# Performance work log

Measured on AMD Instinct MI355X. Metric: run time of the kernel, lower is better.

## Reference

```python
import jax, jax.numpy as jnp
import numpy as np

LMBDA = 1000.0
GAMMA = 1.0  # resolvent_gamma


def setup_inputs() -> dict:
    key = jax.random.key(0)
    k = jax.random.split(key, 6)
    B, K, N, D = 16, 128, 8000, 256
    return {
        "evals_a": jax.random.uniform(k[0], (B, K), dtype=jnp.float32) + 1e-3,
        "pinv_a": jax.random.normal(k[1], (B, K, N), dtype=jnp.float32),
        "descr_a": jax.random.normal(k[2], (B, D, N), dtype=jnp.float32),
        "evals_b": jax.random.uniform(k[3], (B, K), dtype=jnp.float32) + 1e-3,
        "pinv_b": jax.random.normal(k[4], (B, K, N), dtype=jnp.float32),
        "descr_b": jax.random.normal(k[5], (B, D, N), dtype=jnp.float32),
    }


def _compute_mask(evals_a, evals_b, gamma):
    # evals_*: [B, K]. Per-batch normalization by joint max, then resolvent mask.
    scale = jnp.maximum(evals_a.max(axis=-1), evals_b.max(axis=-1))[:, None]
    ga = jnp.power(evals_a / scale, gamma)[:, None, :]  # [B, 1, K]
    gb = jnp.power(evals_b / scale, gamma)[:, :, None]  # [B, K, 1]
    M_re = gb / (gb * gb + 1.0) - ga / (ga * ga + 1.0)
    M_im = 1.0 / (gb * gb + 1.0) - 1.0 / (ga * ga + 1.0)
    return M_re * M_re + M_im * M_im  # [B, K, K]


def _compute_fmap(sdescr_a, sdescr_b, mask, lmbda):
    # sdescr_*: [B, D, K]; mask: [B, K, K]
    AA_aa = jnp.einsum("bdk,bdl->bkl", sdescr_a, sdescr_a)  # [B, K, K]
    AA_ba = jnp.einsum("bdk,bdl->bkl", sdescr_b, sdescr_a)  # [B, K, K]
    K = mask.shape[-1]
    eye = jnp.eye(K, dtype=mask.dtype)
    # Per row i: (AA_aa + lmbda * diag(mask[b, i, :]))^{-1} AA_ba[b, i, :]^T
    A = AA_aa[:, None, :, :] + lmbda * mask[..., None] * eye  # [B, K, K, K]
    Cab = jnp.linalg.solve(A, AA_ba[..., None])[..., 0]  # [B, K, K], row i = solution
    return Cab


def reference(evals_a, pinv_a, descr_a, evals_b, pinv_b, descr_b):
    # spectral descriptor projection: (pinv @ descr^T)^T -> [B, D, K]
    sdescr_a = jnp.einsum("bkn,bdn->bdk", pinv_a, descr_a)
    sdescr_b = jnp.einsum("bkn,bdn->bdk", pinv_b, descr_b)
    mask_ab = _compute_mask(evals_a, evals_b, GAMMA)
    fmap_12 = _compute_fmap(sdescr_a, sdescr_b, mask_ab, LMBDA)
    mask_ba = _compute_mask(evals_b, evals_a, GAMMA)
    fmap_21 = _compute_fmap(sdescr_b, sdescr_a, mask_ba, LMBDA)
    return (fmap_12, fmap_21)
```

## Files before the change

### kernel.cpp

```cpp
#include <hip/hip_runtime.h>

#define BB 16
#define KD 128
#define ND 8000
#define DD 256
#define LMB 1000.0f

typedef __attribute__((ext_vector_type(8))) short bf16x8;
typedef __attribute__((ext_vector_type(4))) short bf16x4;
typedef __attribute__((ext_vector_type(4))) float f32x4;
typedef unsigned short ushort_t;

__device__ inline void split_bf16(float x, ushort_t& h, ushort_t& l) {
    unsigned int bi = __float_as_uint(x);
    h = (ushort_t)(bi >> 16);
    float lo = x - __uint_as_float(bi & 0xFFFF0000u);
    unsigned int lb = __float_as_uint(lo);
    lb = lb + 0x7FFFu + ((lb >> 16) & 1u);
    l = (ushort_t)(lb >> 16);
}

#define PSTR 40

__global__ __launch_bounds__(512, 2) void proj_kernel(
    const float* __restrict__ pinv_a, const float* __restrict__ descr_a,
    const float* __restrict__ pinv_b, const float* __restrict__ descr_b,
    float* __restrict__ sd_a, float* __restrict__ sd_b)
{
    const int b = blockIdx.x, which = blockIdx.y, slice = blockIdx.z;
    const float* P  = (which ? pinv_b  : pinv_a)  + (size_t)b * KD * ND;
    const float* Dm = (which ? descr_b : descr_a) + (size_t)b * DD * ND;
    float* outp = (which ? sd_b : sd_a) + (size_t)b * KD * DD;

    __shared__ ushort_t Ph[KD][PSTR], Pl[KD][PSTR];
    __shared__ ushort_t Dh[DD][PSTR], Dl[DD][PSTR];

    const int tid = threadIdx.x;
    const int lane = tid & 63;
    const int wid = tid >> 6;
    const int wm = wid >> 2, wn = wid & 3;
    const int fr = lane & 15;
    const int kg = lane >> 4;

    f32x4 acc[4][4];
    #pragma unroll
    for (int i = 0; i < 4; ++i)
        #pragma unroll
        for (int j = 0; j < 4; ++j) acc[i][j] = (f32x4){0.f, 0.f, 0.f, 0.f};

    const int n0 = slice * 1000;

    for (int ch = 0; ch < 32; ++ch) {
        const int nb = ch * 32;
        const int valid = (ch == 31) ? 8 : 32;

        #pragma unroll
        for (int u = 0; u < 3; ++u) {
            int row, g;
            const float* src;
            ushort_t (*dsth)[PSTR];
            ushort_t (*dstl)[PSTR];
            if (u == 0) { row = tid >> 2; g = tid & 3; src = P; dsth = Ph; dstl = Pl; }
            else {
                int s2 = tid + (u - 1) * 512;
                row = s2 >> 2; g = s2 & 3; src = Dm; dsth = Dh; dstl = Dl;
            }
            const float* p = src + (size_t)row * ND + n0 + nb + g * 8;
            float4 v0 = {0.f, 0.f, 0.f, 0.f}, v1 = {0.f, 0.f, 0.f, 0.f};
            if (g * 8 < valid)     v0 = *(const float4*)(p);
            if (g * 8 + 4 < valid) v1 = *(const float4*)(p + 4);
            float xs[8] = {v0.x, v0.y, v0.z, v0.w, v1.x, v1.y, v1.z, v1.w};
            bf16x8 hvec, lvec;
            #pragma unroll
            for (int j = 0; j < 8; ++j) {
                ushort_t hh, ll;
                split_bf16(xs[j], hh, ll);
                hvec[j] = (short)hh; lvec[j] = (short)ll;
            }
            *(bf16x8*)(&dsth[row][g * 8]) = hvec;
            *(bf16x8*)(&dstl[row][g * 8]) = lvec;
        }
        __syncthreads();

        bf16x8 Ah[4], Al[4];
        #pragma unroll
        for (int mi = 0; mi < 4; ++mi) {
            int r = wm * 64 + mi * 16 + fr;
            Ah[mi] = *(const bf16x8*)&Ph[r][kg * 8];
            Al[mi] = *(const bf16x8*)&Pl[r][kg * 8];
        }
        #pragma unroll
        for (int ni = 0; ni < 4; ++ni) {
            int c = wn * 64 + ni * 16 + fr;
            bf16x8 Bh = *(const bf16x8*)&Dh[c][kg * 8];
            bf16x8 Bl = *(const bf16x8*)&Dl[c][kg * 8];
            #pragma unroll
            for (int mi = 0; mi < 4; ++mi) {
                acc[mi][ni] = __builtin_amdgcn_mfma_f32_16x16x32_bf16(Ah[mi], Bh, acc[mi][ni], 0, 0, 0);
                acc[mi][ni] = __builtin_amdgcn_mfma_f32_16x16x32_bf16(Ah[mi], Bl, acc[mi][ni], 0, 0, 0);
                acc[mi][ni] = __builtin_amdgcn_mfma_f32_16x16x32_bf16(Al[mi], Bh, acc[mi][ni], 0, 0, 0);
            }
        }
        __syncthreads();
    }

    #pragma unroll
    for (int mi = 0; mi < 4; ++mi)
        #pragma unroll
        for (int ni = 0; ni < 4; ++ni) {
            int rbase = wm * 64 + mi * 16 + kg * 4;
            int ccol  = wn * 64 + ni * 16 + fr;
            #pragma unroll
            for (int r = 0; r < 4; ++r)
                atomicAdd(&outp[(size_t)(rbase + r) * DD + ccol], acc[mi][ni][r]);
        }
}

__global__ __launch_bounds__(256) void mask_kernel(
    const float* __restrict__ ea_g, const float* __restrict__ eb_g,
    float* __restrict__ lm_ab, float* __restrict__ lm_ba)
{
    const int b = blockIdx.x, tid = threadIdx.x;
    __shared__ float ta[KD], ua[KD], tb[KD], ub[KD];
    __shared__ float red[256];
    float e = (tid < KD) ? ea_g[b * KD + tid] : eb_g[b * KD + (tid - KD)];
    red[tid] = e;
    __syncthreads();
    for (int s = 128; s > 0; s >>= 1) {
        if (tid < s) red[tid] = fmaxf(red[tid], red[tid + s]);
        __syncthreads();
    }
    float is = 1.0f / red[0];
    float g = e * is;
    float den = 1.0f / (g * g + 1.0f);
    if (tid < KD) { ta[tid] = g * den; ua[tid] = den; }
    else          { tb[tid - KD] = g * den; ub[tid - KD] = den; }
    __syncthreads();
    for (int idx = tid; idx < KD * KD; idx += 256) {
        int i = idx >> 7, kc = idx & 127;
        float re = tb[i] - ta[kc], im = ub[i] - ua[kc];
        lm_ab[(size_t)b * KD * KD + idx] = LMB * (re * re + im * im);
        float re2 = ta[i] - tb[kc], im2 = ua[i] - ub[kc];
        lm_ba[(size_t)b * KD * KD + idx] = LMB * (re2 * re2 + im2 * im2);
    }
}

#define GSTR 68
__global__ __launch_bounds__(512, 2) void gram_kernel(
    const float* __restrict__ sd_a, const float* __restrict__ sd_b,
    float* __restrict__ AA)
{
    const int b = blockIdx.x, m = blockIdx.y;
    const float* X = (m == 0) ? sd_a : sd_b;
    const float* Y = (m == 2) ? sd_a : X;
    X += (size_t)b * KD * DD;
    Y += (size_t)b * KD * DD;
    float* outp = AA + ((size_t)m * BB + b) * KD * KD;

    __shared__ ushort_t Xh[KD][GSTR], Xl[KD][GSTR];
    __shared__ ushort_t Yh[KD][GSTR], Yl[KD][GSTR];

    const int tid = threadIdx.x;
    const int lane = tid & 63;
    const int wid = tid >> 6;
    const int wm = wid >> 2, wn = wid & 3;
    const int fr = lane & 15;
    const int kg = lane >> 4;

    f32x4 acc[4][2];
    #pragma unroll
    for (int i = 0; i < 4; ++i)
        #pragma unroll
        for (int j = 0; j < 2; ++j) acc[i][j] = (f32x4){0.f, 0.f, 0.f, 0.f};

    for (int d0 = 0; d0 < DD; d0 += 64) {
        #pragma unroll
        for (int u = 0; u < 8; ++u) {
            int idx = tid + (u & 3) * 512;
            int r = idx >> 4, c4 = idx & 15;
            const float* src = (u < 4) ? X : Y;
            float4 v = *(const float4*)(src + (size_t)r * DD + d0 + c4 * 4);
            float xs[4] = {v.x, v.y, v.z, v.w};
            bf16x4 hv, lv;
            #pragma unroll
            for (int q = 0; q < 4; ++q) {
                ushort_t hh, ll;
                split_bf16(xs[q], hh, ll);
                hv[q] = (short)hh; lv[q] = (short)ll;
            }
            if (u < 4) {
                *(bf16x4*)&Xh[r][c4 * 4] = hv;
                *(bf16x4*)&Xl[r][c4 * 4] = lv;
            } else {
                *(bf16x4*)&Yh[r][c4 * 4] = hv;
                *(bf16x4*)&Yl[r][c4 * 4] = lv;
            }
        }
        __syncthreads();

        #pragma unroll
        for (int kk = 0; kk < 2; ++kk) {
            const int co = kk * 32 + kg * 8;
            bf16x8 Ah[4], Al[4];
            #pragma unroll
            for (int mi = 0; mi < 4; ++mi) {
                int r = wm * 64 + mi * 16 + fr;
                Ah[mi] = *(const bf16x8*)&Xh[r][co];
                Al[mi] = *(const bf16x8*)&Xl[r][co];
            }
            #pragma unroll
            for (int ni = 0; ni < 2; ++ni) {
                int c = wn * 32 + ni * 16 + fr;
                bf16x8 Bh = *(const bf16x8*)&Yh[c][co];
                bf16x8 Bl = *(const bf16x8*)&Yl[c][co];
                #pragma unroll
                for (int mi = 0; mi < 4; ++mi) {
                    acc[mi][ni] = __builtin_amdgcn_mfma_f32_16x16x32_bf16(Ah[mi], Bh, acc[mi][ni], 0, 0, 0);
                    acc[mi][ni] = __builtin_amdgcn_mfma_f32_16x16x32_bf16(Ah[mi], Bl, acc[mi][ni], 0, 0, 0);
                    acc[mi][ni] = __builtin_amdgcn_mfma_f32_16x16x32_bf16(Al[mi], Bh, acc[mi][ni], 0, 0, 0);
                }
            }
        }
        __syncthreads();
    }

    #pragma unroll
    for (int mi = 0; mi < 4; ++mi)
        #pragma unroll
        for (int ni = 0; ni < 2; ++ni) {
            int rbase = wm * 64 + mi * 16 + kg * 4;
            int ccol  = wn * 32 + ni * 16 + fr;
            #pragma unroll
            for (int rr = 0; rr < 4; ++rr)
                outp[(size_t)(rbase + rr) * KD + ccol] = acc[mi][ni][rr];
        }
}

__global__ __launch_bounds__(512, 2) void invert_kernel(
    const float* __restrict__ AA, float* __restrict__ Hout)
{
    const int b = blockIdx.x, which = blockIdx.y;
    const float* src = AA + ((size_t)which * BB + b) * KD * KD;
    float* dst = Hout + ((size_t)which * BB + b) * KD * KD;

    __shared__ float rowbuf[2][KD];
    __shared__ float colbuf[2][KD];

    const int tid = threadIdx.x;
    const int rb = tid >> 5;
    const int cg = tid & 31;

    f32x4 Areg[8];
    #pragma unroll
    for (int r = 0; r < 8; ++r)
        Areg[r] = *(const f32x4*)(src + (size_t)(rb * 8 + r) * KD + cg * 4);

    if (rb == 0) *(f32x4*)&rowbuf[0][cg * 4] = Areg[0];
    if (cg == 0) {
        #pragma unroll
        for (int r = 0; r < 8; ++r) colbuf[0][rb * 8 + r] = Areg[r].x;
    }
    __syncthreads();

    for (int j = 0; j < KD; ++j) {
        const int cur = j & 1, nxt = cur ^ 1;
        const int jrb = j >> 3, jr = j & 7, jcg = j >> 2, jc = j & 3;
        const float pv = 1.0f / rowbuf[cur][j];
        const f32x4 orow = *(const f32x4*)&rowbuf[cur][cg * 4];
        const f32x4 prow = orow * pv;
        const bool mycg = (cg == jcg);
        const bool myrb = (rb == jrb);

        #pragma unroll
        for (int r = 0; r < 8; ++r) {
            const float cm = colbuf[cur][rb * 8 + r];
            const float cmul = -cm * pv;
            const bool piv = myrb && (r == jr);
            f32x4 nv;
            nv.x = piv ? prow.x : fmaf(cmul, orow.x, Areg[r].x);
            nv.y = piv ? prow.y : fmaf(cmul, orow.y, Areg[r].y);
            nv.z = piv ? prow.z : fmaf(cmul, orow.z, Areg[r].z);
            nv.w = piv ? prow.w : fmaf(cmul, orow.w, Areg[r].w);
            if (mycg) {
                const float fixv = piv ? pv : cmul;
                nv.x = (jc == 0) ? fixv : nv.x;
                nv.y = (jc == 1) ? fixv : nv.y;
                nv.z = (jc == 2) ? fixv : nv.z;
                nv.w = (jc == 3) ? fixv : nv.w;
            }
            Areg[r] = nv;
        }

        if (j + 1 < KD) {
            const int njrb = (j + 1) >> 3, njr = (j + 1) & 7;
            const int njcg = (j + 1) >> 2, njc = (j + 1) & 3;
            if (rb == njrb) {
                #pragma unroll
                for (int r = 0; r < 8; ++r)
                    if (r == njr) *(f32x4*)&rowbuf[nxt][cg * 4] = Areg[r];
            }
            if (cg == njcg) {
                #pragma unroll
                for (int r = 0; r < 8; ++r) {
                    const f32x4 a = Areg[r];
                    const float e = (njc == 0) ? a.x : (njc == 1) ? a.y : (njc == 2) ? a.z : a.w;
                    colbuf[nxt][rb * 8 + r] = e;
                }
            }
        }
        __syncthreads();
    }

    #pragma unroll
    for (int r = 0; r < 8; ++r)
        *(f32x4*)(dst + (size_t)(rb * 8 + r) * KD + cg * 4) = Areg[r];
}

#define NTERMS 6
__global__ __launch_bounds__(512) void solve_kernel(
    const float* __restrict__ AAba, const float* __restrict__ lm_ab,
    const float* __restrict__ lm_ba, const float* __restrict__ Hmat,
    float* __restrict__ outp)
{
    const int b = blockIdx.x, cg = blockIdx.y, which = blockIdx.z;
    const float* Hm = Hmat + ((size_t)which * BB + b) * KD * KD;
    const float* lm = (which ? lm_ba : lm_ab) + (size_t)b * KD * KD;
    const float* Rs = AAba + (size_t)b * KD * KD;
    float* op = outp + ((size_t)which * BB + b) * KD * KD;
    const int i0 = cg * 32;

    __shared__ float Hs[KD][132];
    __shared__ float Zc[2][32][132];
    __shared__ float lms[32][132];

    const int tid = threadIdx.x;
    const int rq = tid & 31;
    const int cq = tid >> 5;

    #pragma unroll
    for (int u = 0; u < 8; ++u) {
        int idx = tid + u * 512;
        int d = idx >> 5, l4 = idx & 31;
        *(float4*)&Hs[d][l4 * 4] = *(const float4*)(Hm + (size_t)d * KD + l4 * 4);
    }
    #pragma unroll
    for (int u = 0; u < 8; ++u) {
        int idx = tid + u * 512;
        int ic = idx >> 7, l = idx & 127;
        lms[ic][l] = lm[(size_t)(i0 + ic) * KD + l];
    }
    if (which == 0) {
        #pragma unroll
        for (int u = 0; u < 8; ++u) {
            int idx = tid + u * 512;
            int ic = idx >> 7, d = idx & 127;
            Zc[0][ic][d] = Rs[(size_t)(i0 + ic) * KD + d];
        }
    } else {
        #pragma unroll
        for (int u = 0; u < 8; ++u) {
            int idx = tid + u * 512;
            int d = idx >> 5, ic = idx & 31;
            Zc[0][ic][d] = Rs[(size_t)d * KD + i0 + ic];
        }
    }
    __syncthreads();

    float xacc[4][2];
    #pragma unroll
    for (int rr = 0; rr < 4; ++rr) { xacc[rr][0] = 0.f; xacc[rr][1] = 0.f; }
    int cur = 0;
    for (int t = 0; t < NTERMS; ++t) {
        float zr[4][2];
        #pragma unroll
        for (int rr = 0; rr < 4; ++rr) { zr[rr][0] = 0.f; zr[rr][1] = 0.f; }
        #pragma unroll 8
        for (int d4 = 0; d4 < 32; ++d4) {
            float4 hv[4];
            #pragma unroll
            for (int dd = 0; dd < 4; ++dd)
                hv[dd] = *(const float4*)&Hs[d4 * 4 + dd][rq * 4];
            float4 wv[2];
            #pragma unroll
            for (int cc = 0; cc < 2; ++cc)
                wv[cc] = *(const float4*)&Zc[cur][cq * 2 + cc][d4 * 4];
            #pragma unroll
            for (int cc = 0; cc < 2; ++cc) {
                zr[0][cc] += hv[0].x * wv[cc].x + hv[1].x * wv[cc].y + hv[2].x * wv[cc].z + hv[3].x * wv[cc].w;
                zr[1][cc] += hv[0].y * wv[cc].x + hv[1].y * wv[cc].y + hv[2].y * wv[cc].z + hv[3].y * wv[cc].w;
                zr[2][cc] += hv[0].z * wv[cc].x + hv[1].z * wv[cc].y + hv[2].z * wv[cc].z + hv[3].z * wv[cc].w;
                zr[3][cc] += hv[0].w * wv[cc].x + hv[1].w * wv[cc].y + hv[2].w * wv[cc].z + hv[3].w * wv[cc].w;
            }
        }
        const float s = (t & 1) ? -1.f : 1.f;
        #pragma unroll
        for (int rr = 0; rr < 4; ++rr) {
            xacc[rr][0] += s * zr[rr][0];
            xacc[rr][1] += s * zr[rr][1];
        }
        if (t + 1 < NTERMS) {
            #pragma unroll
            for (int cc = 0; cc < 2; ++cc) {
                float4 lmv = *(const float4*)&lms[cq * 2 + cc][rq * 4];
                float4 w;
                w.x = lmv.x * zr[0][cc];
                w.y = lmv.y * zr[1][cc];
                w.z = lmv.z * zr[2][cc];
                w.w = lmv.w * zr[3][cc];
                *(float4*)&Zc[cur ^ 1][cq * 2 + cc][rq * 4] = w;
            }
            __syncthreads();
            cur ^= 1;
        }
    }
    #pragma unroll
    for (int cc = 0; cc < 2; ++cc) {
        float4 o;
        o.x = xacc[0][cc]; o.y = xacc[1][cc]; o.z = xacc[2][cc]; o.w = xacc[3][cc];
        *(float4*)(op + (size_t)(i0 + cq * 2 + cc) * KD + rq * 4) = o;
    }
}

extern "C" void kernel_launch(void* const* d_in, const int* in_sizes, int n_in,
                              void* d_out, int out_size, void* d_ws, size_t ws_size,
                              hipStream_t stream) {
    (void)in_sizes; (void)n_in; (void)out_size; (void)ws_size;
    const float* evals_a = (const float*)d_in[0];
    const float* pinv_a  = (const float*)d_in[1];
    const float* descr_a = (const float*)d_in[2];
    const float* evals_b = (const float*)d_in[3];
    const float* pinv_b  = (const float*)d_in[4];
    const float* descr_b = (const float*)d_in[5];
    float* out = (float*)d_out;
    float* ws = (float*)d_ws;

    const size_t SD = (size_t)BB * KD * DD;
    const size_t MM = (size_t)BB * KD * KD;
    float* sd_a  = ws;
    float* sd_b  = sd_a + SD;
    float* AA    = sd_b + SD;
    float* lm_ab = AA + 3 * MM;
    float* lm_ba = lm_ab + MM;
    float* Hm    = lm_ba + MM;

    hipMemsetAsync(sd_a, 0, 2 * SD * sizeof(float), stream);
    proj_kernel<<<dim3(BB, 2, 8), 512, 0, stream>>>(pinv_a, descr_a, pinv_b, descr_b, sd_a, sd_b);
    mask_kernel<<<dim3(BB), 256, 0, stream>>>(evals_a, evals_b, lm_ab, lm_ba);
    gram_kernel<<<dim3(BB, 3), 512, 0, stream>>>(sd_a, sd_b, AA);
    invert_kernel<<<dim3(BB, 2), 512, 0, stream>>>(AA, Hm);
    solve_kernel<<<dim3(BB, 4, 2), 512, 0, stream>>>(AA + 2 * MM, lm_ab, lm_ba, Hm, out);
}
```

Baseline: 318.6 us.

## Split projection and gram reductions across more blocks with register prefetch

The projection kernel now splits N into 16 slices of 500 instead of 8 of 1000, doubling the grid to 512 blocks, and raises the occupancy hint to 4 blocks per CU. It also prefetches the next chunk's global loads into registers while the MFMAs run on the current chunk. The gram kernel is split over the D dimension into 4 blocks per output that accumulate with atomicAdd, so it launches 192 blocks instead of 48. The memset is widened to zero the gram buffer too. This trades more atomics and register pressure for better GPU fill and overlap of memory and compute.

```diff
diff --git a/kernel.cpp b/kernel.cpp
--- a/kernel.cpp
+++ b/kernel.cpp
@@ -21,8 +21,10 @@
 }
 
 #define PSTR 40
-
-__global__ __launch_bounds__(512, 2) void proj_kernel(
+#define NPS 500
+#define NCHK 16
+
+__global__ __launch_bounds__(512, 4) void proj_kernel(
     const float* __restrict__ pinv_a, const float* __restrict__ descr_a,
     const float* __restrict__ pinv_b, const float* __restrict__ descr_b,
     float* __restrict__ sd_a, float* __restrict__ sd_b)
@@ -41,6 +43,18 @@
     const int wm = wid >> 2, wn = wid & 3;
     const int fr = lane & 15;
     const int kg = lane >> 4;
+    const int n0 = slice * NPS;
+
+    int srow[3], sg[3];
+    const float* sptr[3];
+    {
+        srow[0] = tid >> 2; sg[0] = tid & 3;
+        sptr[0] = P + (size_t)srow[0] * ND + n0 + sg[0] * 8;
+        int s1 = tid;       srow[1] = s1 >> 2; sg[1] = s1 & 3;
+        sptr[1] = Dm + (size_t)srow[1] * ND + n0 + sg[1] * 8;
+        int s2 = tid + 512; srow[2] = s2 >> 2; sg[2] = s2 & 3;
+        sptr[2] = Dm + (size_t)srow[2] * ND + n0 + sg[2] * 8;
+    }
 
     f32x4 acc[4][4];
     #pragma unroll
@@ -48,28 +62,24 @@
         #pragma unroll
         for (int j = 0; j < 4; ++j) acc[i][j] = (f32x4){0.f, 0.f, 0.f, 0.f};
 
-    const int n0 = slice * 1000;
-
-    for (int ch = 0; ch < 32; ++ch) {
-        const int nb = ch * 32;
-        const int valid = (ch == 31) ? 8 : 32;
-
+    float4 pv0, pv1, pv2, pv3, pv4, pv5;
+
+    {
+        const int nb = 0, valid = 32;
+        pv0 = (sg[0] * 8     < valid) ? *(const float4*)(sptr[0] + nb)     : (float4){0,0,0,0};
+        pv1 = (sg[0] * 8 + 4 < valid) ? *(const float4*)(sptr[0] + nb + 4) : (float4){0,0,0,0};
+        pv2 = (sg[1] * 8     < valid) ? *(const float4*)(sptr[1] + nb)     : (float4){0,0,0,0};
+        pv3 = (sg[1] * 8 + 4 < valid) ? *(const float4*)(sptr[1] + nb + 4) : (float4){0,0,0,0};
+        pv4 = (sg[2] * 8     < valid) ? *(const float4*)(sptr[2] + nb)     : (float4){0,0,0,0};
+        pv5 = (sg[2] * 8 + 4 < valid) ? *(const float4*)(sptr[2] + nb + 4) : (float4){0,0,0,0};
+    }
+
+    for (int ch = 0; ch < NCHK; ++ch) {
         #pragma unroll
         for (int u = 0; u < 3; ++u) {
-            int row, g;
-            const float* src;
-            ushort_t (*dsth)[PSTR];
-            ushort_t (*dstl)[PSTR];
-            if (u == 0) { row = tid >> 2; g = tid & 3; src = P; dsth = Ph; dstl = Pl; }
-            else {
-                int s2 = tid + (u - 1) * 512;
-                row = s2 >> 2; g = s2 & 3; src = Dm; dsth = Dh; dstl = Dl;
-            }
-            const float* p = src + (size_t)row * ND + n0 + nb + g * 8;
-            float4 v0 = {0.f, 0.f, 0.f, 0.f}, v1 = {0.f, 0.f, 0.f, 0.f};
-            if (g * 8 < valid)     v0 = *(const float4*)(p);
-            if (g * 8 + 4 < valid) v1 = *(const float4*)(p + 4);
-            float xs[8] = {v0.x, v0.y, v0.z, v0.w, v1.x, v1.y, v1.z, v1.w};
+            float4 a = (u == 0) ? pv0 : (u == 1) ? pv2 : pv4;
+            float4 c = (u == 0) ? pv1 : (u == 1) ? pv3 : pv5;
+            float xs[8] = {a.x, a.y, a.z, a.w, c.x, c.y, c.z, c.w};
             bf16x8 hvec, lvec;
             #pragma unroll
             for (int j = 0; j < 8; ++j) {
@@ -77,10 +87,23 @@
                 split_bf16(xs[j], hh, ll);
                 hvec[j] = (short)hh; lvec[j] = (short)ll;
             }
-            *(bf16x8*)(&dsth[row][g * 8]) = hvec;
-            *(bf16x8*)(&dstl[row][g * 8]) = lvec;
+            ushort_t* dh = (u == 0) ? &Ph[srow[0]][sg[0] * 8] : &Dh[srow[u]][sg[u] * 8];
+            ushort_t* dl = (u == 0) ? &Pl[srow[0]][sg[0] * 8] : &Dl[srow[u]][sg[u] * 8];
+            *(bf16x8*)dh = hvec;
+            *(bf16x8*)dl = lvec;
         }
         __syncthreads();
+
+        if (ch + 1 < NCHK) {
+            const int nb = (ch + 1) * 32;
+            const int valid = (ch + 1 == NCHK - 1) ? (NPS - 32 * (NCHK - 1)) : 32;
+            pv0 = (sg[0] * 8     < valid) ? *(const float4*)(sptr[0] + nb)     : (float4){0,0,0,0};
+            pv1 = (sg[0] * 8 + 4 < valid) ? *(const float4*)(sptr[0] + nb + 4) : (float4){0,0,0,0};
+            pv2 = (sg[1] * 8     < valid) ? *(const float4*)(sptr[1] + nb)     : (float4){0,0,0,0};
+            pv3 = (sg[1] * 8 + 4 < valid) ? *(const float4*)(sptr[1] + nb + 4) : (float4){0,0,0,0};
+            pv4 = (sg[2] * 8     < valid) ? *(const float4*)(sptr[2] + nb)     : (float4){0,0,0,0};
+            pv5 = (sg[2] * 8 + 4 < valid) ? *(const float4*)(sptr[2] + nb + 4) : (float4){0,0,0,0};
+        }
 
         bf16x8 Ah[4], Al[4];
         #pragma unroll
@@ -150,12 +173,13 @@
     const float* __restrict__ sd_a, const float* __restrict__ sd_b,
     float* __restrict__ AA)
 {
-    const int b = blockIdx.x, m = blockIdx.y;
+    const int b = blockIdx.x, m = blockIdx.y, dchunk = blockIdx.z;
     const float* X = (m == 0) ? sd_a : sd_b;
     const float* Y = (m == 2) ? sd_a : X;
     X += (size_t)b * KD * DD;
     Y += (size_t)b * KD * DD;
     float* outp = AA + ((size_t)m * BB + b) * KD * KD;
+    const int d0 = dchunk * 64;
 
     __shared__ ushort_t Xh[KD][GSTR], Xl[KD][GSTR];
     __shared__ ushort_t Yh[KD][GSTR], Yl[KD][GSTR];
@@ -173,55 +197,52 @@
         #pragma unroll
         for (int j = 0; j < 2; ++j) acc[i][j] = (f32x4){0.f, 0.f, 0.f, 0.f};
 
-    for (int d0 = 0; d0 < DD; d0 += 64) {
-        #pragma unroll
-        for (int u = 0; u < 8; ++u) {
-            int idx = tid + (u & 3) * 512;
-            int r = idx >> 4, c4 = idx & 15;
-            const float* src = (u < 4) ? X : Y;
-            float4 v = *(const float4*)(src + (size_t)r * DD + d0 + c4 * 4);
-            float xs[4] = {v.x, v.y, v.z, v.w};
-            bf16x4 hv, lv;
-            #pragma unroll
-            for (int q = 0; q < 4; ++q) {
-                ushort_t hh, ll;
-                split_bf16(xs[q], hh, ll);
-                hv[q] = (short)hh; lv[q] = (short)ll;
-            }
-            if (u < 4) {
-                *(bf16x4*)&Xh[r][c4 * 4] = hv;
-                *(bf16x4*)&Xl[r][c4 * 4] = lv;
-            } else {
-                *(bf16x4*)&Yh[r][c4 * 4] = hv;
-                *(bf16x4*)&Yl[r][c4 * 4] = lv;
-            }
-        }
-        __syncthreads();
-
-        #pragma unroll
-        for (int kk = 0; kk < 2; ++kk) {
-            const int co = kk * 32 + kg * 8;
-            bf16x8 Ah[4], Al[4];
+    #pragma unroll
+    for (int u = 0; u < 8; ++u) {
+        int idx = tid + (u & 3) * 512;
+        int r = idx >> 4, c4 = idx & 15;
+        const float* src = (u < 4) ? X : Y;
+        float4 v = *(const float4*)(src + (size_t)r * DD + d0 + c4 * 4);
+        float xs[4] = {v.x, v.y, v.z, v.w};
+        bf16x4 hv, lv;
+        #pragma unroll
+        for (int q = 0; q < 4; ++q) {
+            ushort_t hh, ll;
+            split_bf16(xs[q], hh, ll);
+            hv[q] = (short)hh; lv[q] = (short)ll;
+        }
+        if (u < 4) {
+            *(bf16x4*)&Xh[r][c4 * 4] = hv;
+            *(bf16x4*)&Xl[r][c4 * 4] = lv;
+        } else {
+            *(bf16x4*)&Yh[r][c4 * 4] = hv;
+            *(bf16x4*)&Yl[r][c4 * 4] = lv;
+        }
+    }
+    __syncthreads();
+
+    #pragma unroll
+    for (int kk = 0; kk < 2; ++kk) {
+        const int co = kk * 32 + kg * 8;
+        bf16x8 Ah[4], Al[4];
+        #pragma unroll
+        for (int mi = 0; mi < 4; ++mi) {
+            int r = wm * 64 + mi * 16 + fr;
+            Ah[mi] = *(const bf16x8*)&Xh[r][co];
+            Al[mi] = *(const bf16x8*)&Xl[r][co];
+        }
+        #pragma unroll
+        for (int ni = 0; ni < 2; ++ni) {
+            int c = wn * 32 + ni * 16 + fr;
+            bf16x8 Bh = *(const bf16x8*)&Yh[c][co];
+            bf16x8 Bl = *(const bf16x8*)&Yl[c][co];
             #pragma unroll
             for (int mi = 0; mi < 4; ++mi) {
-                int r = wm * 64 + mi * 16 + fr;
-                Ah[mi] = *(const bf16x8*)&Xh[r][co];
-                Al[mi] = *(const bf16x8*)&Xl[r][co];
-            }
-            #pragma unroll
-            for (int ni = 0; ni < 2; ++ni) {
-                int c = wn * 32 + ni * 16 + fr;
-                bf16x8 Bh = *(const bf16x8*)&Yh[c][co];
-                bf16x8 Bl = *(const bf16x8*)&Yl[c][co];
-                #pragma unroll
-                for (int mi = 0; mi < 4; ++mi) {
-                    acc[mi][ni] = __builtin_amdgcn_mfma_f32_16x16x32_bf16(Ah[mi], Bh, acc[mi][ni], 0, 0, 0);
-                    acc[mi][ni] = __builtin_amdgcn_mfma_f32_16x16x32_bf16(Ah[mi], Bl, acc[mi][ni], 0, 0, 0);
-                    acc[mi][ni] = __builtin_amdgcn_mfma_f32_16x16x32_bf16(Al[mi], Bh, acc[mi][ni], 0, 0, 0);
-                }
-            }
-        }
-        __syncthreads();
+                acc[mi][ni] = __builtin_amdgcn_mfma_f32_16x16x32_bf16(Ah[mi], Bh, acc[mi][ni], 0, 0, 0);
+                acc[mi][ni] = __builtin_amdgcn_mfma_f32_16x16x32_bf16(Ah[mi], Bl, acc[mi][ni], 0, 0, 0);
+                acc[mi][ni] = __builtin_amdgcn_mfma_f32_16x16x32_bf16(Al[mi], Bh, acc[mi][ni], 0, 0, 0);
+            }
+        }
     }
 
     #pragma unroll
@@ -232,7 +253,7 @@
             int ccol  = wn * 32 + ni * 16 + fr;
             #pragma unroll
             for (int rr = 0; rr < 4; ++rr)
-                outp[(size_t)(rbase + rr) * KD + ccol] = acc[mi][ni][rr];
+                atomicAdd(&outp[(size_t)(rbase + rr) * KD + ccol], acc[mi][ni][rr]);
         }
 }
 
@@ -443,10 +464,10 @@
     float* lm_ba = lm_ab + MM;
     float* Hm    = lm_ba + MM;
 
-    hipMemsetAsync(sd_a, 0, 2 * SD * sizeof(float), stream);
-    proj_kernel<<<dim3(BB, 2, 8), 512, 0, stream>>>(pinv_a, descr_a, pinv_b, descr_b, sd_a, sd_b);
+    hipMemsetAsync(sd_a, 0, (2 * SD + 3 * MM) * sizeof(float), stream);
+    proj_kernel<<<dim3(BB, 2, 16), 512, 0, stream>>>(pinv_a, descr_a, pinv_b, descr_b, sd_a, sd_b);
     mask_kernel<<<dim3(BB), 256, 0, stream>>>(evals_a, evals_b, lm_ab, lm_ba);
-    gram_kernel<<<dim3(BB, 3), 512, 0, stream>>>(sd_a, sd_b, AA);
+    gram_kernel<<<dim3(BB, 3, 4), 512, 0, stream>>>(sd_a, sd_b, AA);
     invert_kernel<<<dim3(BB, 2), 512, 0, stream>>>(AA, Hm);
     solve_kernel<<<dim3(BB, 4, 2), 512, 0, stream>>>(AA + 2 * MM, lm_ab, lm_ba, Hm, out);
 }
```

Result: slower. 327.7 us (+2.9%).

## Pipeline projection GEMM with async global-to-LDS loads and split gram over D

Applied to the files above, without the earlier changes.

The projection kernel now uses 1024-thread blocks that stream raw fp32 tiles into double-buffered, XOR-swizzled LDS through global_load_lds, overlapping the next chunk's load with the current chunk's MFMA work. The bf16 hi/lo split moves from the load stage to just after the LDS read. N is split into 25 slices instead of 8 to spread work over more blocks. The gram kernel is also split across four D-chunks, accumulating with atomics into a buffer the widened memset now zeroes, which adds atomic traffic and repeated conversion work in exchange for more parallelism.

```diff
diff --git a/kernel.cpp b/kernel.cpp
--- a/kernel.cpp
+++ b/kernel.cpp
@@ -11,7 +11,7 @@
 typedef __attribute__((ext_vector_type(4))) float f32x4;
 typedef unsigned short ushort_t;
 
-__device__ inline void split_bf16(float x, ushort_t& h, ushort_t& l) {
+__device__ __forceinline__ void split_bf16(float x, ushort_t& h, ushort_t& l) {
     unsigned int bi = __float_as_uint(x);
     h = (ushort_t)(bi >> 16);
     float lo = x - __uint_as_float(bi & 0xFFFF0000u);
@@ -20,9 +20,29 @@
     l = (ushort_t)(lb >> 16);
 }
 
-#define PSTR 40
-
-__global__ __launch_bounds__(512, 2) void proj_kernel(
+__device__ __forceinline__ void cvt8(f32x4 a, f32x4 b, bf16x8& h, bf16x8& l) {
+    #pragma unroll
+    for (int j = 0; j < 4; ++j) {
+        ushort_t hh, ll;
+        split_bf16(a[j], hh, ll); h[j] = (short)hh; l[j] = (short)ll;
+        split_bf16(b[j], hh, ll); h[4 + j] = (short)hh; l[4 + j] = (short)ll;
+    }
+}
+
+__device__ __forceinline__ void gll16(const float* g, float* l) {
+    __builtin_amdgcn_global_load_lds(
+        (const __attribute__((address_space(1))) void*)g,
+        (__attribute__((address_space(3))) void*)l, 16, 0, 0);
+}
+
+#define ROWS 384
+#define CHF 32
+#define NPS 320
+#define NCHK 10
+#define SBUF_FL 12288
+
+__global__ __attribute__((amdgpu_flat_work_group_size(1024, 1024), amdgpu_waves_per_eu(2, 4)))
+void proj_kernel(
     const float* __restrict__ pinv_a, const float* __restrict__ descr_a,
     const float* __restrict__ pinv_b, const float* __restrict__ descr_b,
     float* __restrict__ sd_a, float* __restrict__ sd_b)
@@ -32,8 +52,7 @@
     const float* Dm = (which ? descr_b : descr_a) + (size_t)b * DD * ND;
     float* outp = (which ? sd_b : sd_a) + (size_t)b * KD * DD;
 
-    __shared__ ushort_t Ph[KD][PSTR], Pl[KD][PSTR];
-    __shared__ ushort_t Dh[DD][PSTR], Dl[DD][PSTR];
+    __shared__ float Sbuf[2][SBUF_FL];
 
     const int tid = threadIdx.x;
     const int lane = tid & 63;
@@ -41,74 +60,75 @@
     const int wm = wid >> 2, wn = wid & 3;
     const int fr = lane & 15;
     const int kg = lane >> 4;
-
-    f32x4 acc[4][4];
-    #pragma unroll
-    for (int i = 0; i < 4; ++i)
+    const int n0 = slice * NPS;
+
+    const float* gp[3];
+    int lof[3];
+    #pragma unroll
+    for (int u = 0; u < 3; ++u) {
+        int I = wid * 3 + u;
+        int r = I * 8 + (lane >> 3);
+        int c4 = (lane & 7) ^ (r & 7);
+        const float* rowp = (r < KD) ? (P + (size_t)r * ND) : (Dm + (size_t)(r - KD) * ND);
+        gp[u] = rowp + n0 + c4 * 4;
+        lof[u] = I * 256;
+    }
+
+    f32x4 acc[2][4];
+    #pragma unroll
+    for (int i = 0; i < 2; ++i)
         #pragma unroll
         for (int j = 0; j < 4; ++j) acc[i][j] = (f32x4){0.f, 0.f, 0.f, 0.f};
 
-    const int n0 = slice * 1000;
-
-    for (int ch = 0; ch < 32; ++ch) {
-        const int nb = ch * 32;
-        const int valid = (ch == 31) ? 8 : 32;
-
-        #pragma unroll
-        for (int u = 0; u < 3; ++u) {
-            int row, g;
-            const float* src;
-            ushort_t (*dsth)[PSTR];
-            ushort_t (*dstl)[PSTR];
-            if (u == 0) { row = tid >> 2; g = tid & 3; src = P; dsth = Ph; dstl = Pl; }
-            else {
-                int s2 = tid + (u - 1) * 512;
-                row = s2 >> 2; g = s2 & 3; src = Dm; dsth = Dh; dstl = Dl;
-            }
-            const float* p = src + (size_t)row * ND + n0 + nb + g * 8;
-            float4 v0 = {0.f, 0.f, 0.f, 0.f}, v1 = {0.f, 0.f, 0.f, 0.f};
-            if (g * 8 < valid)     v0 = *(const float4*)(p);
-            if (g * 8 + 4 < valid) v1 = *(const float4*)(p + 4);
-            float xs[8] = {v0.x, v0.y, v0.z, v0.w, v1.x, v1.y, v1.z, v1.w};
-            bf16x8 hvec, lvec;
-            #pragma unroll
-            for (int j = 0; j < 8; ++j) {
-                ushort_t hh, ll;
-                split_bf16(xs[j], hh, ll);
-                hvec[j] = (short)hh; lvec[j] = (short)ll;
-            }
-            *(bf16x8*)(&dsth[row][g * 8]) = hvec;
-            *(bf16x8*)(&dstl[row][g * 8]) = lvec;
-        }
-        __syncthreads();
-
-        bf16x8 Ah[4], Al[4];
-        #pragma unroll
-        for (int mi = 0; mi < 4; ++mi) {
-            int r = wm * 64 + mi * 16 + fr;
-            Ah[mi] = *(const bf16x8*)&Ph[r][kg * 8];
-            Al[mi] = *(const bf16x8*)&Pl[r][kg * 8];
-        }
+    #pragma unroll
+    for (int u = 0; u < 3; ++u) gll16(gp[u], &Sbuf[0][lof[u]]);
+
+    for (int t = 0; t < NCHK; ++t) {
+        const int buf = t & 1;
+        if (t + 1 < NCHK) {
+            #pragma unroll
+            for (int u = 0; u < 3; ++u) gll16(gp[u] + (t + 1) * CHF, &Sbuf[buf ^ 1][lof[u]]);
+            __builtin_amdgcn_sched_barrier(0);
+            asm volatile("s_waitcnt vmcnt(3)" ::: "memory");
+        } else {
+            __builtin_amdgcn_sched_barrier(0);
+            asm volatile("s_waitcnt vmcnt(0)" ::: "memory");
+        }
+        __builtin_amdgcn_sched_barrier(0);
+        __builtin_amdgcn_s_barrier();
+        __builtin_amdgcn_sched_barrier(0);
+
+        const float* base = &Sbuf[buf][0];
         #pragma unroll
         for (int ni = 0; ni < 4; ++ni) {
-            int c = wn * 64 + ni * 16 + fr;
-            bf16x8 Bh = *(const bf16x8*)&Dh[c][kg * 8];
-            bf16x8 Bl = *(const bf16x8*)&Dl[c][kg * 8];
-            #pragma unroll
-            for (int mi = 0; mi < 4; ++mi) {
-                acc[mi][ni] = __builtin_amdgcn_mfma_f32_16x16x32_bf16(Ah[mi], Bh, acc[mi][ni], 0, 0, 0);
-                acc[mi][ni] = __builtin_amdgcn_mfma_f32_16x16x32_bf16(Ah[mi], Bl, acc[mi][ni], 0, 0, 0);
-                acc[mi][ni] = __builtin_amdgcn_mfma_f32_16x16x32_bf16(Al[mi], Bh, acc[mi][ni], 0, 0, 0);
-            }
-        }
-        __syncthreads();
-    }
-
-    #pragma unroll
-    for (int mi = 0; mi < 4; ++mi)
+            const int rB = KD + wn * 64 + ni * 16 + fr;
+            const int rb7 = rB & 7;
+            f32x4 b0 = *(const f32x4*)(base + rB * CHF + (((2 * kg)     ^ rb7) << 2));
+            f32x4 b1 = *(const f32x4*)(base + rB * CHF + (((2 * kg + 1) ^ rb7) << 2));
+            bf16x8 Bh, Bl;
+            cvt8(b0, b1, Bh, Bl);
+            #pragma unroll
+            for (int mi = 0; mi < 2; ++mi) {
+                const int rA = wm * 32 + mi * 16 + fr;
+                const int ra7 = rA & 7;
+                f32x4 a0 = *(const f32x4*)(base + rA * CHF + (((2 * kg)     ^ ra7) << 2));
+                f32x4 a1 = *(const f32x4*)(base + rA * CHF + (((2 * kg + 1) ^ ra7) << 2));
+                bf16x8 Ah, Al;
+                cvt8(a0, a1, Ah, Al);
+                acc[mi][ni] = __builtin_amdgcn_mfma_f32_16x16x32_bf16(Ah, Bh, acc[mi][ni], 0, 0, 0);
+                acc[mi][ni] = __builtin_amdgcn_mfma_f32_16x16x32_bf16(Ah, Bl, acc[mi][ni], 0, 0, 0);
+                acc[mi][ni] = __builtin_amdgcn_mfma_f32_16x16x32_bf16(Al, Bh, acc[mi][ni], 0, 0, 0);
+            }
+        }
+        __builtin_amdgcn_sched_barrier(0);
+        __builtin_amdgcn_s_barrier();
+    }
+
+    #pragma unroll
+    for (int mi = 0; mi < 2; ++mi)
         #pragma unroll
         for (int ni = 0; ni < 4; ++ni) {
-            int rbase = wm * 64 + mi * 16 + kg * 4;
+            int rbase = wm * 32 + mi * 16 + kg * 4;
             int ccol  = wn * 64 + ni * 16 + fr;
             #pragma unroll
             for (int r = 0; r < 4; ++r)
@@ -150,12 +170,13 @@
     const float* __restrict__ sd_a, const float* __restrict__ sd_b,
     float* __restrict__ AA)
 {
-    const int b = blockIdx.x, m = blockIdx.y;
+    const int b = blockIdx.x, m = blockIdx.y, dchunk = blockIdx.z;
     const float* X = (m == 0) ? sd_a : sd_b;
     const float* Y = (m == 2) ? sd_a : X;
     X += (size_t)b * KD * DD;
     Y += (size_t)b * KD * DD;
     float* outp = AA + ((size_t)m * BB + b) * KD * KD;
+    const int d0 = dchunk * 64;
 
     __shared__ ushort_t Xh[KD][GSTR], Xl[KD][GSTR];
     __shared__ ushort_t Yh[KD][GSTR], Yl[KD][GSTR];
@@ -173,55 +194,52 @@
         #pragma unroll
         for (int j = 0; j < 2; ++j) acc[i][j] = (f32x4){0.f, 0.f, 0.f, 0.f};
 
-    for (int d0 = 0; d0 < DD; d0 += 64) {
-        #pragma unroll
-        for (int u = 0; u < 8; ++u) {
-            int idx = tid + (u & 3) * 512;
-            int r = idx >> 4, c4 = idx & 15;
-            const float* src = (u < 4) ? X : Y;
-            float4 v = *(const float4*)(src + (size_t)r * DD + d0 + c4 * 4);
-            float xs[4] = {v.x, v.y, v.z, v.w};
-            bf16x4 hv, lv;
-            #pragma unroll
-            for (int q = 0; q < 4; ++q) {
-                ushort_t hh, ll;
-                split_bf16(xs[q], hh, ll);
-                hv[q] = (short)hh; lv[q] = (short)ll;
-            }
-            if (u < 4) {
-                *(bf16x4*)&Xh[r][c4 * 4] = hv;
-                *(bf16x4*)&Xl[r][c4 * 4] = lv;
-            } else {
-                *(bf16x4*)&Yh[r][c4 * 4] = hv;
-                *(bf16x4*)&Yl[r][c4 * 4] = lv;
-            }
-        }
-        __syncthreads();
-
-        #pragma unroll
-        for (int kk = 0; kk < 2; ++kk) {
-            const int co = kk * 32 + kg * 8;
-            bf16x8 Ah[4], Al[4];
+    #pragma unroll
+    for (int u = 0; u < 8; ++u) {
+        int idx = tid + (u & 3) * 512;
+        int r = idx >> 4, c4 = idx & 15;
+        const float* src = (u < 4) ? X : Y;
+        float4 v = *(const float4*)(src + (size_t)r * DD + d0 + c4 * 4);
+        float xs[4] = {v.x, v.y, v.z, v.w};
+        bf16x4 hv, lv;
+        #pragma unroll
+        for (int q = 0; q < 4; ++q) {
+            ushort_t hh, ll;
+            split_bf16(xs[q], hh, ll);
+            hv[q] = (short)hh; lv[q] = (short)ll;
+        }
+        if (u < 4) {
+            *(bf16x4*)&Xh[r][c4 * 4] = hv;
+            *(bf16x4*)&Xl[r][c4 * 4] = lv;
+        } else {
+            *(bf16x4*)&Yh[r][c4 * 4] = hv;
+            *(bf16x4*)&Yl[r][c4 * 4] = lv;
+        }
+    }
+    __syncthreads();
+
+    #pragma unroll
+    for (int kk = 0; kk < 2; ++kk) {
+        const int co = kk * 32 + kg * 8;
+        bf16x8 Ah[4], Al[4];
+        #pragma unroll
+        for (int mi = 0; mi < 4; ++mi) {
+            int r = wm * 64 + mi * 16 + fr;
+            Ah[mi] = *(const bf16x8*)&Xh[r][co];
+            Al[mi] = *(const bf16x8*)&Xl[r][co];
+        }
+        #pragma unroll
+        for (int ni = 0; ni < 2; ++ni) {
+            int c = wn * 32 + ni * 16 + fr;
+            bf16x8 Bh = *(const bf16x8*)&Yh[c][co];
+            bf16x8 Bl = *(const bf16x8*)&Yl[c][co];
             #pragma unroll
             for (int mi = 0; mi < 4; ++mi) {
-                int r = wm * 64 + mi * 16 + fr;
-                Ah[mi] = *(const bf16x8*)&Xh[r][co];
-                Al[mi] = *(const bf16x8*)&Xl[r][co];
-            }
-            #pragma unroll
-            for (int ni = 0; ni < 2; ++ni) {
-                int c = wn * 32 + ni * 16 + fr;
-                bf16x8 Bh = *(const bf16x8*)&Yh[c][co];
-                bf16x8 Bl = *(const bf16x8*)&Yl[c][co];
-                #pragma unroll
-                for (int mi = 0; mi < 4; ++mi) {
-                    acc[mi][ni] = __builtin_amdgcn_mfma_f32_16x16x32_bf16(Ah[mi], Bh, acc[mi][ni], 0, 0, 0);
-                    acc[mi][ni] = __builtin_amdgcn_mfma_f32_16x16x32_bf16(Ah[mi], Bl, acc[mi][ni], 0, 0, 0);
-                    acc[mi][ni] = __builtin_amdgcn_mfma_f32_16x16x32_bf16(Al[mi], Bh, acc[mi][ni], 0, 0, 0);
-                }
-            }
-        }
-        __syncthreads();
+                acc[mi][ni] = __builtin_amdgcn_mfma_f32_16x16x32_bf16(Ah[mi], Bh, acc[mi][ni], 0, 0, 0);
+                acc[mi][ni] = __builtin_amdgcn_mfma_f32_16x16x32_bf16(Ah[mi], Bl, acc[mi][ni], 0, 0, 0);
+                acc[mi][ni] = __builtin_amdgcn_mfma_f32_16x16x32_bf16(Al[mi], Bh, acc[mi][ni], 0, 0, 0);
+            }
+        }
     }
 
     #pragma unroll
@@ -232,7 +250,7 @@
             int ccol  = wn * 32 + ni * 16 + fr;
             #pragma unroll
             for (int rr = 0; rr < 4; ++rr)
-                outp[(size_t)(rbase + rr) * KD + ccol] = acc[mi][ni][rr];
+                atomicAdd(&outp[(size_t)(rbase + rr) * KD + ccol], acc[mi][ni][rr]);
         }
 }
 
@@ -443,10 +461,10 @@
     float* lm_ba = lm_ab + MM;
     float* Hm    = lm_ba + MM;
 
-    hipMemsetAsync(sd_a, 0, 2 * SD * sizeof(float), stream);
-    proj_kernel<<<dim3(BB, 2, 8), 512, 0, stream>>>(pinv_a, descr_a, pinv_b, descr_b, sd_a, sd_b);
+    hipMemsetAsync(sd_a, 0, (2 * SD + 3 * MM) * sizeof(float), stream);
+    proj_kernel<<<dim3(BB, 2, 25), 1024, 0, stream>>>(pinv_a, descr_a, pinv_b, descr_b, sd_a, sd_b);
     mask_kernel<<<dim3(BB), 256, 0, stream>>>(evals_a, evals_b, lm_ab, lm_ba);
-    gram_kernel<<<dim3(BB, 3), 512, 0, stream>>>(sd_a, sd_b, AA);
+    gram_kernel<<<dim3(BB, 3, 4), 512, 0, stream>>>(sd_a, sd_b, AA);
     invert_kernel<<<dim3(BB, 2), 512, 0, stream>>>(AA, Hm);
     solve_kernel<<<dim3(BB, 4, 2), 512, 0, stream>>>(AA + 2 * MM, lm_ab, lm_ba, Hm, out);
 }
```

New measurement: 376.7 us. 1.18x slower.
